# Kernel optimization log

Hardware: AMD Instinct MI355X
Metric: run time of the kernel (lower is better)

## Reference

```python
import jax, jax.numpy as jnp
import numpy as np

OBS_DIM, HIDDEN, OUT = 64, 128, 128
BATCH = 524288


def _mlp(x, W1, b1, W2, b2, W3, b3):
    # torch Linear: y = x @ W.T + b
    h = jax.nn.relu(x @ W1.T + b1)
    h = jax.nn.relu(h @ W2.T + b2)
    return h @ W3.T + b3


def setup_inputs() -> dict:
    key = jax.random.key(0)
    ks = jax.random.split(key, 13)

    def lin(k, fan_out, fan_in):
        bound = 1.0 / np.sqrt(fan_in)
        kw, kb = jax.random.split(k)
        W = jax.random.uniform(kw, (fan_out, fan_in), jnp.float32, -bound, bound)
        b = jax.random.uniform(kb, (fan_out,), jnp.float32, -bound, bound)
        return W, b

    tW1, tb1 = lin(ks[0], HIDDEN, OBS_DIM)
    tW2, tb2 = lin(ks[1], HIDDEN, HIDDEN)
    tW3, tb3 = lin(ks[2], OUT, HIDDEN)
    pW1, pb1 = lin(ks[3], HIDDEN, OBS_DIM)
    pW2, pb2 = lin(ks[4], HIDDEN, HIDDEN)
    pW3, pb3 = lin(ks[5], OUT, HIDDEN)
    obs = jax.random.normal(ks[6], (BATCH, OBS_DIM), jnp.float32)
    return {
        "obs": obs,
        "reward_mean": jnp.zeros((1,), jnp.float32),
        "reward_m2": jnp.zeros((1,), jnp.float32),
        "reward_count": jnp.zeros((1,), jnp.float32),
        "tW1": tW1, "tb1": tb1, "tW2": tW2, "tb2": tb2, "tW3": tW3, "tb3": tb3,
        "pW1": pW1, "pb1": pb1, "pW2": pW2, "pb2": pb2, "pW3": pW3, "pb3": pb3,
    }


def reference(obs, reward_mean, reward_m2, reward_count,
              tW1, tb1, tW2, tb2, tW3, tb3,
              pW1, pb1, pW2, pb2, pW3, pb3):
    # compute_bonus: per-sample MSE between fixed target net and predictor net
    tgt = _mlp(obs, tW1, tb1, tW2, tb2, tW3, tb3)
    pred = _mlp(obs, pW1, pb1, pW2, pb2, pW3, pb3)
    rewards = jnp.mean((tgt - pred) ** 2, axis=-1)  # (batch,)

    # normalize_rewards: sequential Welford over every element ==
    # single batch Welford + Chan merge with running stats (exact same math)
    n = jnp.float32(rewards.shape[0])
    batch_mean = jnp.mean(rewards)
    batch_m2 = jnp.sum((rewards - batch_mean) ** 2)
    new_count = reward_count + n                      # (1,)
    delta = batch_mean - reward_mean                  # (1,)
    new_mean = reward_mean + delta * n / new_count
    new_m2 = reward_m2 + batch_m2 + delta * delta * reward_count * n / new_count
    std = jnp.where(new_count > 1.0,
                    jnp.sqrt(new_m2 / (new_count - 1.0)),
                    jnp.ones_like(new_mean))
    normalized = (rewards - new_mean) / (std + 1e-8)  # (batch,)
    return normalized
```

## Files before the change

kernel.cpp:

```cpp
#include <hip/hip_runtime.h>
#include <stdint.h>

#define BATCH 524288
#define OBSD  64

typedef short v8s __attribute__((ext_vector_type(8)));
typedef float v4f __attribute__((ext_vector_type(4)));

union U8 { int4 i4; v8s v; uint32_t u[4]; };

__device__ __forceinline__ uint32_t pk2(float a, float b) {
  uint32_t r;
  asm("v_cvt_pk_bf16_f32 %0, %1, %2" : "=v"(r) : "v"(a), "v"(b));
  return r;
}

__device__ __forceinline__ void glds16(const uint16_t* g, uint16_t* l) {
  __builtin_amdgcn_global_load_lds(
      (const __attribute__((address_space(1))) uint32_t*)g,
      (__attribute__((address_space(3))) uint32_t*)l, 16, 0, 0);
}

__global__ void rnd_prep(const float* __restrict__ tW1, const float* __restrict__ tW2,
                         const float* __restrict__ tW3, const float* __restrict__ pW1,
                         const float* __restrict__ pW2, const float* __restrict__ pW3,
                         uint16_t* __restrict__ Wall, float* __restrict__ sums) {
  int g = blockIdx.x * 256 + threadIdx.x;
  if (g < 2) sums[g] = 0.0f;
  const float* src;
  uint16_t* dst;
  float sgn = 1.f;
  if (g < 2048) {
    int u = g;
    int m = u >> 10; u &= 1023;
    int rt = u >> 7, ks = (u >> 6) & 1, lane = u & 63;
    int n = lane & 15, qq = lane >> 4;
    src = (m ? pW1 : tW1) + (rt * 16 + n) * 64 + ks * 32 + qq * 8;
    dst = Wall + m * 8192 + u * 8;
  } else if (g < 6144) {
    int u = g - 2048;
    int m = u >> 11; u &= 2047;
    int rt = u >> 8, ks = (u >> 6) & 3, lane = u & 63;
    int n = lane & 15, qq = lane >> 4;
    src = (m ? pW2 : tW2) + (rt * 16 + n) * 128 + ks * 32 + qq * 8;
    dst = Wall + 16384 + m * 16384 + u * 8;
  } else {
    int u = g - 6144;
    int m = u >> 11; u &= 2047;
    int rt = u >> 8, ks = (u >> 6) & 3, lane = u & 63;
    int n = lane & 15, qq = lane >> 4;
    src = (m ? pW3 : tW3) + (rt * 16 + n) * 128 + ks * 32 + qq * 8;
    sgn = m ? -1.f : 1.f;
    dst = Wall + 49152 + m * 16384 + u * 8;
  }
  float4 f0 = *(const float4*)src, f1 = *(const float4*)(src + 4);
  U8 u8;
  u8.u[0] = pk2(sgn * f0.x, sgn * f0.y); u8.u[1] = pk2(sgn * f0.z, sgn * f0.w);
  u8.u[2] = pk2(sgn * f1.x, sgn * f1.y); u8.u[3] = pk2(sgn * f1.z, sgn * f1.w);
  *(int4*)dst = u8.i4;
}

__global__ __launch_bounds__(256, 2) void rnd_main(
    const float* __restrict__ obs, const uint16_t* __restrict__ Wall,
    const float* __restrict__ b1t, const float* __restrict__ b2t,
    const float* __restrict__ b1p, const float* __restrict__ b2p,
    const float* __restrict__ b3t, const float* __restrict__ b3p,
    float* __restrict__ rewards, float* __restrict__ sums) {
  extern __shared__ __align__(16) uint16_t Wl[];
  const int t    = threadIdx.x;
  const int lane = t & 63;
  const int wv   = t >> 6;
  const int n    = lane & 15;
  const int q    = lane >> 4;
  const int s0   = (blockIdx.x * 4 + wv) * 64;

  const uint16_t* gsrc = Wall + wv * 2048 + lane * 8;
  uint16_t*       lbas = Wl + wv * 2048;
  auto stage = [&](int chunkElemOff, int bufByteOff) {
    #pragma unroll
    for (int j = 0; j < 4; ++j)
      glds16(gsrc + chunkElemOff + j * 512, lbas + bufByteOff / 2 + j * 512);
  };

  const uint16_t* rb = Wl + lane * 8;
  float* Bl = (float*)(Wl + 24576);

  stage(0, 0);
  stage(16384, 16384);
  stage(24576, 32768);
  {
    int i = t;
    #pragma unroll
    for (int it = 0; it < 3; ++it, i += 256)
      if (i < 640) {
        int seg = i >> 7, off = i & 127;
        float v;
        if (seg == 0) v = b1t[off];
        else if (seg == 1) v = b2t[off];
        else if (seg == 2) v = b1p[off];
        else if (seg == 3) v = b2p[off];
        else v = b3t[off] - b3p[off];
        Bl[i] = v;
      }
  }
  float4 of[16];
  #pragma unroll
  for (int ct = 0; ct < 4; ++ct)
    #pragma unroll
    for (int ks = 0; ks < 2; ++ks) {
      const float* p = obs + (size_t)(s0 + ct * 16 + n) * OBSD + ks * 32 + q * 8;
      of[(ct * 2 + ks) * 2 + 0] = *(const float4*)p;
      of[(ct * 2 + ks) * 2 + 1] = *(const float4*)(p + 4);
    }
  v8s obf[4][2];
  #pragma unroll
  for (int ct = 0; ct < 4; ++ct)
    #pragma unroll
    for (int ks = 0; ks < 2; ++ks) {
      float4 f0 = of[(ct * 2 + ks) * 2 + 0];
      float4 f1 = of[(ct * 2 + ks) * 2 + 1];
      U8 u;
      u.u[0] = pk2(f0.x, f0.y); u.u[1] = pk2(f0.z, f0.w);
      u.u[2] = pk2(f1.x, f1.y); u.u[3] = pk2(f1.z, f1.w);
      obf[ct][ks] = u.v;
    }

  auto bias4 = [&](int bbase, int rtBase, v4f (&a)[4][4]) {
    #pragma unroll
    for (int r = 0; r < 4; ++r) {
      v4f c = *(const v4f*)(Bl + bbase + (rtBase + r) * 16 + q * 4);
      #pragma unroll
      for (int ct = 0; ct < 4; ++ct) a[r][ct] = c;
    }
  };
  auto pack4 = [&](v4f (&a)[4][4], v8s (&BF)[4][4], int ksBase) {
    uint32_t P[4][4][2];
    #pragma unroll
    for (int r = 0; r < 4; ++r)
      #pragma unroll
      for (int ct = 0; ct < 4; ++ct) {
        v4f v = a[r][ct];
        v[0] = fmaxf(v[0], 0.f); v[1] = fmaxf(v[1], 0.f);
        v[2] = fmaxf(v[2], 0.f); v[3] = fmaxf(v[3], 0.f);
        P[r][ct][0] = pk2(v[0], v[1]);
        P[r][ct][1] = pk2(v[2], v[3]);
      }
    #pragma unroll
    for (int kk = 0; kk < 2; ++kk)
      #pragma unroll
      for (int ct = 0; ct < 4; ++ct) {
        uint32_t x0 = P[2 * kk][ct][0],     x1 = P[2 * kk][ct][1];
        uint32_t y0 = P[2 * kk + 1][ct][0], y1 = P[2 * kk + 1][ct][1];
        asm("v_permlane32_swap_b32 %0, %1" : "+v"(x0), "+v"(y0));
        asm("v_permlane16_swap_b32 %0, %1" : "+v"(x0), "+v"(y0));
        asm("v_permlane32_swap_b32 %0, %1" : "+v"(x1), "+v"(y1));
        asm("v_permlane16_swap_b32 %0, %1" : "+v"(x1), "+v"(y1));
        U8 u; u.u[0] = x0; u.u[1] = x1; u.u[2] = y0; u.u[3] = y1;
        BF[ksBase + kk][ct] = u.v;
      }
  };
  auto layer1 = [&](int bbase, v8s (&BF)[4][4]) {
    v4f a[4][4];
    bias4(bbase, 0, a);
    __builtin_amdgcn_s_setprio(1);
    #pragma unroll
    for (int ks = 0; ks < 2; ++ks)
      #pragma unroll
      for (int r = 0; r < 4; ++r) {
        U8 u; u.i4 = *(const int4*)(rb + (r * 2 + ks) * 512);
        #pragma unroll
        for (int ct = 0; ct < 4; ++ct)
          a[r][ct] = __builtin_amdgcn_mfma_f32_16x16x32_bf16(u.v, obf[ct][ks], a[r][ct], 0, 0, 0);
      }
    __builtin_amdgcn_s_setprio(0);
    pack4(a, BF, 0);
    bias4(bbase, 4, a);
    __builtin_amdgcn_s_setprio(1);
    #pragma unroll
    for (int ks = 0; ks < 2; ++ks)
      #pragma unroll
      for (int r = 0; r < 4; ++r) {
        U8 u; u.i4 = *(const int4*)(rb + ((r + 4) * 2 + ks) * 512);
        #pragma unroll
        for (int ct = 0; ct < 4; ++ct)
          a[r][ct] = __builtin_amdgcn_mfma_f32_16x16x32_bf16(u.v, obf[ct][ks], a[r][ct], 0, 0, 0);
      }
    __builtin_amdgcn_s_setprio(0);
    pack4(a, BF, 2);
  };
  auto halfmm = [&](int bufOff, v8s (&BFin)[4][4], v4f (&a)[4][4]) {
    __builtin_amdgcn_s_setprio(1);
    #pragma unroll
    for (int ks = 0; ks < 4; ++ks)
      #pragma unroll
      for (int r = 0; r < 4; ++r) {
        U8 u; u.i4 = *(const int4*)(rb + bufOff / 2 + (r * 4 + ks) * 512);
        #pragma unroll
        for (int ct = 0; ct < 4; ++ct)
          a[r][ct] = __builtin_amdgcn_mfma_f32_16x16x32_bf16(u.v, BFin[ks][ct], a[r][ct], 0, 0, 0);
      }
    __builtin_amdgcn_s_setprio(0);
  };

  v8s BF1[4][4], BF2t[4][4], BF2p[4][4];

  __syncthreads();
  layer1(0, BF1);
  __syncthreads(); stage(8192, 0);
  { v4f a[4][4]; bias4(128, 0, a); halfmm(16384, BF1, a); pack4(a, BF2t, 0); }
  __syncthreads(); stage(32768, 16384);
  { v4f a[4][4]; bias4(128, 4, a); halfmm(32768, BF1, a); pack4(a, BF2t, 2); }
  __syncthreads(); stage(40960, 32768);
  layer1(256, BF1);
  __syncthreads(); stage(49152, 0);
  { v4f a[4][4]; bias4(384, 0, a); halfmm(16384, BF1, a); pack4(a, BF2p, 0); }
  __syncthreads(); stage(65536, 16384);
  { v4f a[4][4]; bias4(384, 4, a); halfmm(32768, BF1, a); pack4(a, BF2p, 2); }
  __syncthreads(); stage(57344, 32768);

  float p[4] = {0.f, 0.f, 0.f, 0.f};
  {
    v4f a[4][4];
    #pragma unroll
    for (int r = 0; r < 4; ++r) {
      v4f c = *(const v4f*)(Bl + 512 + r * 16 + q * 4);
      #pragma unroll
      for (int ct = 0; ct < 4; ++ct) a[r][ct] = c;
    }
    halfmm(0, BF2t, a);
    __syncthreads(); stage(73728, 0);
    halfmm(16384, BF2p, a);
    #pragma unroll
    for (int r = 0; r < 4; ++r)
      #pragma unroll
      for (int ct = 0; ct < 4; ++ct) {
        v4f v = a[r][ct];
        p[ct] += v[0]*v[0] + v[1]*v[1] + v[2]*v[2] + v[3]*v[3];
      }
  }
  __syncthreads();
  {
    v4f a[4][4];
    #pragma unroll
    for (int r = 0; r < 4; ++r) {
      v4f c = *(const v4f*)(Bl + 512 + (r + 4) * 16 + q * 4);
      #pragma unroll
      for (int ct = 0; ct < 4; ++ct) a[r][ct] = c;
    }
    halfmm(32768, BF2t, a);
    halfmm(0, BF2p, a);
    #pragma unroll
    for (int r = 0; r < 4; ++r)
      #pragma unroll
      for (int ct = 0; ct < 4; ++ct) {
        v4f v = a[r][ct];
        p[ct] += v[0]*v[0] + v[1]*v[1] + v[2]*v[2] + v[3]*v[3];
      }
  }

  float r[4];
  #pragma unroll
  for (int ct = 0; ct < 4; ++ct) {
    p[ct] += __shfl_xor(p[ct], 32);
    p[ct] += __shfl_xor(p[ct], 16);
    r[ct] = p[ct] * (1.0f / 128.0f);
  }
  if (q == 0) {
    #pragma unroll
    for (int ct = 0; ct < 4; ++ct) rewards[s0 + ct * 16 + n] = r[ct];
  }
  float s  = r[0] + r[1] + r[2] + r[3];
  float ss = r[0]*r[0] + r[1]*r[1] + r[2]*r[2] + r[3]*r[3];
  s  += __shfl_xor(s, 8);  s  += __shfl_xor(s, 4);  s  += __shfl_xor(s, 2);  s  += __shfl_xor(s, 1);
  ss += __shfl_xor(ss, 8); ss += __shfl_xor(ss, 4); ss += __shfl_xor(ss, 2); ss += __shfl_xor(ss, 1);
  __syncthreads();
  float* red = (float*)Wl;
  if (lane == 0) { red[wv] = s; red[8 + wv] = ss; }
  __syncthreads();
  if (t == 0) {
    atomicAdd(&sums[0], red[0] + red[1] + red[2] + red[3]);
    atomicAdd(&sums[1], red[8] + red[9] + red[10] + red[11]);
  }
}

__global__ void rnd_norm(const float* __restrict__ rewards, const float* __restrict__ sums,
                         const float* __restrict__ rm, const float* __restrict__ rm2,
                         const float* __restrict__ rc, float* __restrict__ out) {
  float S = sums[0], SS = sums[1];
  float nb = (float)BATCH;
  float bm = S / nb;
  float bm2 = SS - nb * bm * bm;
  float cnt = rc[0];
  float newc = cnt + nb;
  float delta = bm - rm[0];
  float newmean = rm[0] + delta * nb / newc;
  float newm2 = rm2[0] + bm2 + delta * delta * cnt * nb / newc;
  float sd = (newc > 1.f) ? sqrtf(newm2 / (newc - 1.f)) : 1.f;
  float inv = 1.f / (sd + 1e-8f);
  int i = (blockIdx.x * 256 + threadIdx.x) * 4;
  float4 r = *(const float4*)(rewards + i);
  float4 o;
  o.x = (r.x - newmean) * inv; o.y = (r.y - newmean) * inv;
  o.z = (r.z - newmean) * inv; o.w = (r.w - newmean) * inv;
  *(float4*)(out + i) = o;
}

extern "C" void kernel_launch(void* const* d_in, const int* in_sizes, int n_in,
                              void* d_out, int out_size, void* d_ws, size_t ws_size,
                              hipStream_t stream) {
  const float* obs = (const float*)d_in[0];
  const float* rm  = (const float*)d_in[1];
  const float* rm2 = (const float*)d_in[2];
  const float* rc  = (const float*)d_in[3];
  const float* tW1 = (const float*)d_in[4];
  const float* tb1 = (const float*)d_in[5];
  const float* tW2 = (const float*)d_in[6];
  const float* tb2 = (const float*)d_in[7];
  const float* tW3 = (const float*)d_in[8];
  const float* tb3 = (const float*)d_in[9];
  const float* pW1 = (const float*)d_in[10];
  const float* pb1 = (const float*)d_in[11];
  const float* pW2 = (const float*)d_in[12];
  const float* pb2 = (const float*)d_in[13];
  const float* pW3 = (const float*)d_in[14];
  const float* pb3 = (const float*)d_in[15];

  float*    sums    = (float*)d_ws;
  float*    rewards = (float*)((char*)d_ws + 256);
  uint16_t* Wall    = (uint16_t*)((char*)d_ws + 256 + (size_t)BATCH * 4);

  (void)hipFuncSetAttribute((const void*)rnd_main,
                            hipFuncAttributeMaxDynamicSharedMemorySize, 51712);

  rnd_prep<<<40, 256, 0, stream>>>(tW1, tW2, tW3, pW1, pW2, pW3, Wall, sums);
  rnd_main<<<BATCH / 256, 256, 51712, stream>>>(obs, Wall, tb1, tb2, pb1, pb2,
                                                tb3, pb3, rewards, sums);
  rnd_norm<<<BATCH / 1024, 256, 0, stream>>>(rewards, sums, rm, rm2, rc, (float*)d_out);
}
```

Before: 272.8 us.

## Give each wave private double-buffered weight stages synced by waitcnt

Replaces the block-shared weight staging and __syncthreads barriers with per-wave private LDS regions. Each wave streams every weight chunk itself into a two-slot ping-pong buffer and waits with s_waitcnt vmcnt/lgkmcnt instead of a block barrier. The aim is to remove barrier stalls between waves and overlap each chunk's global-to-LDS load with the MFMA work on the previous chunk. The cost is that each wave loads all weights itself, which means four times the redundant L2 traffic and more LDS per block (68 KB), and that may limit occupancy.

```diff
diff --git a/kernel.cpp b/kernel.cpp
--- a/kernel.cpp
+++ b/kernel.cpp
@@ -20,6 +20,10 @@
       (const __attribute__((address_space(1))) uint32_t*)g,
       (__attribute__((address_space(3))) uint32_t*)l, 16, 0, 0);
 }
+
+#define PH_GUARD() asm volatile("s_waitcnt lgkmcnt(0)" ::: "memory")
+#define PH_WAIT8() asm volatile("s_waitcnt vmcnt(8)" ::: "memory")
+#define PH_WAIT0() asm volatile("s_waitcnt vmcnt(0)" ::: "memory")
 
 __global__ void rnd_prep(const float* __restrict__ tW1, const float* __restrict__ tW2,
                          const float* __restrict__ tW3, const float* __restrict__ pW1,
@@ -74,20 +78,18 @@
   const int q    = lane >> 4;
   const int s0   = (blockIdx.x * 4 + wv) * 64;
 
-  const uint16_t* gsrc = Wall + wv * 2048 + lane * 8;
-  uint16_t*       lbas = Wl + wv * 2048;
-  auto stage = [&](int chunkElemOff, int bufByteOff) {
-    #pragma unroll
-    for (int j = 0; j < 4; ++j)
-      glds16(gsrc + chunkElemOff + j * 512, lbas + bufByteOff / 2 + j * 512);
-  };
-
-  const uint16_t* rb = Wl + lane * 8;
-  float* Bl = (float*)(Wl + 24576);
-
-  stage(0, 0);
-  stage(16384, 16384);
-  stage(24576, 32768);
+  const uint16_t* gsrc = Wall + lane * 8;
+  uint16_t*       lwb  = Wl + wv * 8192;
+  auto stageh = [&](int hcOff, int par) {
+    uint16_t* d = lwb + par * 4096;
+    #pragma unroll
+    for (int j = 0; j < 8; ++j)
+      glds16(gsrc + hcOff + j * 512, d + j * 512);
+  };
+  const uint16_t* rbw = Wl + wv * 8192 + lane * 8;
+  float* Bl = (float*)(Wl + 32768);
+
+  stageh(0, 0);
   {
     int i = t;
     #pragma unroll
@@ -133,6 +135,14 @@
       for (int ct = 0; ct < 4; ++ct) a[r][ct] = c;
     }
   };
+  auto bias2 = [&](int rB, int bR, v4f (&a)[4][4]) {
+    #pragma unroll
+    for (int r = 0; r < 2; ++r) {
+      v4f c = *(const v4f*)(Bl + 512 + (bR + r) * 16 + q * 4);
+      #pragma unroll
+      for (int ct = 0; ct < 4; ++ct) a[rB + r][ct] = c;
+    }
+  };
   auto pack4 = [&](v4f (&a)[4][4], v8s (&BF)[4][4], int ksBase) {
     uint32_t P[4][4][2];
     #pragma unroll
@@ -159,104 +169,91 @@
         BF[ksBase + kk][ct] = u.v;
       }
   };
-  auto layer1 = [&](int bbase, v8s (&BF)[4][4]) {
+  auto l1h = [&](int par, int bbase, int rtB, v8s (&BF)[4][4]) {
     v4f a[4][4];
-    bias4(bbase, 0, a);
+    bias4(bbase, rtB, a);
     __builtin_amdgcn_s_setprio(1);
     #pragma unroll
     for (int ks = 0; ks < 2; ++ks)
       #pragma unroll
       for (int r = 0; r < 4; ++r) {
-        U8 u; u.i4 = *(const int4*)(rb + (r * 2 + ks) * 512);
+        U8 u; u.i4 = *(const int4*)(rbw + par * 4096 + (r * 2 + ks) * 512);
         #pragma unroll
         for (int ct = 0; ct < 4; ++ct)
           a[r][ct] = __builtin_amdgcn_mfma_f32_16x16x32_bf16(u.v, obf[ct][ks], a[r][ct], 0, 0, 0);
       }
     __builtin_amdgcn_s_setprio(0);
-    pack4(a, BF, 0);
-    bias4(bbase, 4, a);
+    pack4(a, BF, rtB >> 1);
+  };
+  auto mm2r = [&](int par, int rB, v8s (&BFin)[4][4], v4f (&a)[4][4]) {
     __builtin_amdgcn_s_setprio(1);
     #pragma unroll
-    for (int ks = 0; ks < 2; ++ks)
-      #pragma unroll
-      for (int r = 0; r < 4; ++r) {
-        U8 u; u.i4 = *(const int4*)(rb + ((r + 4) * 2 + ks) * 512);
+    for (int rr = 0; rr < 2; ++rr)
+      #pragma unroll
+      for (int ks = 0; ks < 4; ++ks) {
+        U8 u; u.i4 = *(const int4*)(rbw + par * 4096 + (rr * 4 + ks) * 512);
         #pragma unroll
         for (int ct = 0; ct < 4; ++ct)
-          a[r][ct] = __builtin_amdgcn_mfma_f32_16x16x32_bf16(u.v, obf[ct][ks], a[r][ct], 0, 0, 0);
+          a[rB + rr][ct] = __builtin_amdgcn_mfma_f32_16x16x32_bf16(u.v, BFin[ks][ct], a[rB + rr][ct], 0, 0, 0);
       }
     __builtin_amdgcn_s_setprio(0);
-    pack4(a, BF, 2);
-  };
-  auto halfmm = [&](int bufOff, v8s (&BFin)[4][4], v4f (&a)[4][4]) {
-    __builtin_amdgcn_s_setprio(1);
-    #pragma unroll
-    for (int ks = 0; ks < 4; ++ks)
-      #pragma unroll
-      for (int r = 0; r < 4; ++r) {
-        U8 u; u.i4 = *(const int4*)(rb + bufOff / 2 + (r * 4 + ks) * 512);
-        #pragma unroll
-        for (int ct = 0; ct < 4; ++ct)
-          a[r][ct] = __builtin_amdgcn_mfma_f32_16x16x32_bf16(u.v, BFin[ks][ct], a[r][ct], 0, 0, 0);
-      }
-    __builtin_amdgcn_s_setprio(0);
+  };
+  float p[4] = {0.f, 0.f, 0.f, 0.f};
+  v4f a2[4][4];
+  auto reduce4 = [&]() {
+    #pragma unroll
+    for (int r = 0; r < 4; ++r)
+      #pragma unroll
+      for (int ct = 0; ct < 4; ++ct) {
+        v4f v = a2[r][ct];
+        p[ct] += v[0]*v[0] + v[1]*v[1] + v[2]*v[2] + v[3]*v[3];
+      }
   };
 
   v8s BF1[4][4], BF2t[4][4], BF2p[4][4];
 
   __syncthreads();
-  layer1(0, BF1);
-  __syncthreads(); stage(8192, 0);
-  { v4f a[4][4]; bias4(128, 0, a); halfmm(16384, BF1, a); pack4(a, BF2t, 0); }
-  __syncthreads(); stage(32768, 16384);
-  { v4f a[4][4]; bias4(128, 4, a); halfmm(32768, BF1, a); pack4(a, BF2t, 2); }
-  __syncthreads(); stage(40960, 32768);
-  layer1(256, BF1);
-  __syncthreads(); stage(49152, 0);
-  { v4f a[4][4]; bias4(384, 0, a); halfmm(16384, BF1, a); pack4(a, BF2p, 0); }
-  __syncthreads(); stage(65536, 16384);
-  { v4f a[4][4]; bias4(384, 4, a); halfmm(32768, BF1, a); pack4(a, BF2p, 2); }
-  __syncthreads(); stage(57344, 32768);
-
-  float p[4] = {0.f, 0.f, 0.f, 0.f};
-  {
-    v4f a[4][4];
-    #pragma unroll
-    for (int r = 0; r < 4; ++r) {
-      v4f c = *(const v4f*)(Bl + 512 + r * 16 + q * 4);
-      #pragma unroll
-      for (int ct = 0; ct < 4; ++ct) a[r][ct] = c;
-    }
-    halfmm(0, BF2t, a);
-    __syncthreads(); stage(73728, 0);
-    halfmm(16384, BF2p, a);
-    #pragma unroll
-    for (int r = 0; r < 4; ++r)
-      #pragma unroll
-      for (int ct = 0; ct < 4; ++ct) {
-        v4f v = a[r][ct];
-        p[ct] += v[0]*v[0] + v[1]*v[1] + v[2]*v[2] + v[3]*v[3];
-      }
-  }
-  __syncthreads();
-  {
-    v4f a[4][4];
-    #pragma unroll
-    for (int r = 0; r < 4; ++r) {
-      v4f c = *(const v4f*)(Bl + 512 + (r + 4) * 16 + q * 4);
-      #pragma unroll
-      for (int ct = 0; ct < 4; ++ct) a[r][ct] = c;
-    }
-    halfmm(32768, BF2t, a);
-    halfmm(0, BF2p, a);
-    #pragma unroll
-    for (int r = 0; r < 4; ++r)
-      #pragma unroll
-      for (int ct = 0; ct < 4; ++ct) {
-        v4f v = a[r][ct];
-        p[ct] += v[0]*v[0] + v[1]*v[1] + v[2]*v[2] + v[3]*v[3];
-      }
-  }
+
+  PH_GUARD(); stageh(4096, 1);  PH_WAIT8();
+  l1h(0, 0, 0, BF1);
+  PH_GUARD(); stageh(16384, 0); PH_WAIT8();
+  l1h(1, 0, 4, BF1);
+  PH_GUARD(); stageh(20480, 1); PH_WAIT8();
+  bias4(128, 0, a2); mm2r(0, 0, BF1, a2);
+  PH_GUARD(); stageh(24576, 0); PH_WAIT8();
+  mm2r(1, 2, BF1, a2); pack4(a2, BF2t, 0);
+  PH_GUARD(); stageh(28672, 1); PH_WAIT8();
+  bias4(128, 4, a2); mm2r(0, 0, BF1, a2);
+  PH_GUARD(); stageh(8192, 0);  PH_WAIT8();
+  mm2r(1, 2, BF1, a2); pack4(a2, BF2t, 2);
+  PH_GUARD(); stageh(12288, 1); PH_WAIT8();
+  l1h(0, 256, 0, BF1);
+  PH_GUARD(); stageh(32768, 0); PH_WAIT8();
+  l1h(1, 256, 4, BF1);
+  PH_GUARD(); stageh(36864, 1); PH_WAIT8();
+  bias4(384, 0, a2); mm2r(0, 0, BF1, a2);
+  PH_GUARD(); stageh(40960, 0); PH_WAIT8();
+  mm2r(1, 2, BF1, a2); pack4(a2, BF2p, 0);
+  PH_GUARD(); stageh(45056, 1); PH_WAIT8();
+  bias4(384, 4, a2); mm2r(0, 0, BF1, a2);
+  PH_GUARD(); stageh(49152, 0); PH_WAIT8();
+  mm2r(1, 2, BF1, a2); pack4(a2, BF2p, 2);
+  PH_GUARD(); stageh(53248, 1); PH_WAIT8();
+  bias2(0, 0, a2); mm2r(0, 0, BF2t, a2);
+  PH_GUARD(); stageh(65536, 0); PH_WAIT8();
+  bias2(2, 2, a2); mm2r(1, 2, BF2t, a2);
+  PH_GUARD(); stageh(69632, 1); PH_WAIT8();
+  mm2r(0, 0, BF2p, a2);
+  PH_GUARD(); stageh(57344, 0); PH_WAIT8();
+  mm2r(1, 2, BF2p, a2); reduce4();
+  PH_GUARD(); stageh(61440, 1); PH_WAIT8();
+  bias2(0, 4, a2); mm2r(0, 0, BF2t, a2);
+  PH_GUARD(); stageh(73728, 0); PH_WAIT8();
+  bias2(2, 6, a2); mm2r(1, 2, BF2t, a2);
+  PH_GUARD(); stageh(77824, 1); PH_WAIT8();
+  mm2r(0, 0, BF2p, a2);
+  PH_WAIT0();
+  mm2r(1, 2, BF2p, a2); reduce4();
 
   float r[4];
   #pragma unroll
@@ -330,10 +327,10 @@
   uint16_t* Wall    = (uint16_t*)((char*)d_ws + 256 + (size_t)BATCH * 4);
 
   (void)hipFuncSetAttribute((const void*)rnd_main,
-                            hipFuncAttributeMaxDynamicSharedMemorySize, 51712);
+                            hipFuncAttributeMaxDynamicSharedMemorySize, 68096);
 
   rnd_prep<<<40, 256, 0, stream>>>(tW1, tW2, tW3, pW1, pW2, pW3, Wall, sums);
-  rnd_main<<<BATCH / 256, 256, 51712, stream>>>(obs, Wall, tb1, tb2, pb1, pb2,
+  rnd_main<<<BATCH / 256, 256, 68096, stream>>>(obs, Wall, tb1, tb2, pb1, pb2,
                                                 tb3, pb3, rewards, sums);
   rnd_norm<<<BATCH / 1024, 256, 0, stream>>>(rewards, sums, rm, rm2, rc, (float*)d_out);
 }
```

Measured after the change: 285.0 us. 1.04x slower.

## Add fourth LDS weight buffer and restructure staging to halve barriers

Applied to the files above, without the earlier changes.

Grows the LDS weight ring from three to four 16KB buffers so predictor layer-1 weights are staged up front. The layer-2 and layer-3 schedule is reordered so two chunks are staged per barrier, which cuts the number of __syncthreads and gives global-to-LDS loads more time to land behind MFMA work. pack4 is deferred past the barrier to overlap with the staging. The cost is more LDS per block (about 66KB versus about 50KB), which may reduce how many blocks fit per CU.

```diff
diff --git a/kernel.cpp b/kernel.cpp
--- a/kernel.cpp
+++ b/kernel.cpp
@@ -83,11 +83,12 @@
   };
 
   const uint16_t* rb = Wl + lane * 8;
-  float* Bl = (float*)(Wl + 24576);
+  float* Bl = (float*)(Wl + 32768);
 
   stage(0, 0);
   stage(16384, 16384);
   stage(24576, 32768);
+  stage(8192, 49152);
   {
     int i = t;
     #pragma unroll
@@ -159,7 +160,7 @@
         BF[ksBase + kk][ct] = u.v;
       }
   };
-  auto layer1 = [&](int bbase, v8s (&BF)[4][4]) {
+  auto layer1 = [&](int bufOff, int bbase, v8s (&BF)[4][4]) {
     v4f a[4][4];
     bias4(bbase, 0, a);
     __builtin_amdgcn_s_setprio(1);
@@ -167,7 +168,7 @@
     for (int ks = 0; ks < 2; ++ks)
       #pragma unroll
       for (int r = 0; r < 4; ++r) {
-        U8 u; u.i4 = *(const int4*)(rb + (r * 2 + ks) * 512);
+        U8 u; u.i4 = *(const int4*)(rb + bufOff / 2 + (r * 2 + ks) * 512);
         #pragma unroll
         for (int ct = 0; ct < 4; ++ct)
           a[r][ct] = __builtin_amdgcn_mfma_f32_16x16x32_bf16(u.v, obf[ct][ks], a[r][ct], 0, 0, 0);
@@ -180,7 +181,7 @@
     for (int ks = 0; ks < 2; ++ks)
       #pragma unroll
       for (int r = 0; r < 4; ++r) {
-        U8 u; u.i4 = *(const int4*)(rb + ((r + 4) * 2 + ks) * 512);
+        U8 u; u.i4 = *(const int4*)(rb + bufOff / 2 + ((r + 4) * 2 + ks) * 512);
         #pragma unroll
         for (int ct = 0; ct < 4; ++ct)
           a[r][ct] = __builtin_amdgcn_mfma_f32_16x16x32_bf16(u.v, obf[ct][ks], a[r][ct], 0, 0, 0);
@@ -203,20 +204,25 @@
   };
 
   v8s BF1[4][4], BF2t[4][4], BF2p[4][4];
-
-  __syncthreads();
-  layer1(0, BF1);
-  __syncthreads(); stage(8192, 0);
-  { v4f a[4][4]; bias4(128, 0, a); halfmm(16384, BF1, a); pack4(a, BF2t, 0); }
-  __syncthreads(); stage(32768, 16384);
-  { v4f a[4][4]; bias4(128, 4, a); halfmm(32768, BF1, a); pack4(a, BF2t, 2); }
-  __syncthreads(); stage(40960, 32768);
-  layer1(256, BF1);
-  __syncthreads(); stage(49152, 0);
-  { v4f a[4][4]; bias4(384, 0, a); halfmm(16384, BF1, a); pack4(a, BF2p, 0); }
-  __syncthreads(); stage(65536, 16384);
-  { v4f a[4][4]; bias4(384, 4, a); halfmm(32768, BF1, a); pack4(a, BF2p, 2); }
-  __syncthreads(); stage(57344, 32768);
+  v4f a2[4][4];
+
+  __syncthreads();
+  layer1(0, 0, BF1);
+  bias4(128, 0, a2); halfmm(16384, BF1, a2);
+  __syncthreads();
+  stage(32768, 0); stage(40960, 16384);
+  pack4(a2, BF2t, 0);
+  bias4(128, 4, a2); halfmm(32768, BF1, a2);
+  layer1(49152, 256, BF1);
+  __syncthreads();
+  stage(49152, 32768); stage(65536, 49152);
+  pack4(a2, BF2t, 2);
+  bias4(384, 0, a2); halfmm(0, BF1, a2);
+  pack4(a2, BF2p, 0);
+  bias4(384, 4, a2); halfmm(16384, BF1, a2);
+  __syncthreads();
+  stage(57344, 0); stage(73728, 16384);
+  pack4(a2, BF2p, 2);
 
   float p[4] = {0.f, 0.f, 0.f, 0.f};
   {
@@ -227,9 +233,8 @@
       #pragma unroll
       for (int ct = 0; ct < 4; ++ct) a[r][ct] = c;
     }
-    halfmm(0, BF2t, a);
-    __syncthreads(); stage(73728, 0);
-    halfmm(16384, BF2p, a);
+    halfmm(32768, BF2t, a);
+    halfmm(49152, BF2p, a);
     #pragma unroll
     for (int r = 0; r < 4; ++r)
       #pragma unroll
@@ -247,8 +252,8 @@
       #pragma unroll
       for (int ct = 0; ct < 4; ++ct) a[r][ct] = c;
     }
-    halfmm(32768, BF2t, a);
-    halfmm(0, BF2p, a);
+    halfmm(0, BF2t, a);
+    halfmm(16384, BF2p, a);
     #pragma unroll
     for (int r = 0; r < 4; ++r)
       #pragma unroll
@@ -330,10 +335,10 @@
   uint16_t* Wall    = (uint16_t*)((char*)d_ws + 256 + (size_t)BATCH * 4);
 
   (void)hipFuncSetAttribute((const void*)rnd_main,
-                            hipFuncAttributeMaxDynamicSharedMemorySize, 51712);
+                            hipFuncAttributeMaxDynamicSharedMemorySize, 68096);
 
   rnd_prep<<<40, 256, 0, stream>>>(tW1, tW2, tW3, pW1, pW2, pW3, Wall, sums);
-  rnd_main<<<BATCH / 256, 256, 51712, stream>>>(obs, Wall, tb1, tb2, pb1, pb2,
+  rnd_main<<<BATCH / 256, 256, 68096, stream>>>(obs, Wall, tb1, tb2, pb1, pb2,
                                                 tb3, pb3, rewards, sums);
   rnd_norm<<<BATCH / 1024, 256, 0, stream>>>(rewards, sums, rm, rm2, rc, (float*)d_out);
 }
```

New measurement: 269.8 us. About the same (-1.1%).
